# Performance work log

Hardware: AMD Instinct MI355X
Metric: run time of the kernel (lower is better)

The kernel has to match this reference:

```python
import jax, jax.numpy as jnp
import numpy as np

VARIANCES = jnp.array([0.1, 0.1, 0.2, 0.2], jnp.float32)
MAX_TOTAL = 200       # max_total_size
MAX_PER_CLASS = 50    # per-class NMS cap (combined-NMS max_output_size_per_class)
IOU_THR = 0.5
SCORE_THR = 0.5       # score_threshold
EPS = 1e-8


def setup_inputs() -> dict:
    key = jax.random.key(0)
    k1, k2, kc, kh = jax.random.split(key, 4)
    B, N, C = 16, 24564, 81
    pred_deltas = jax.random.normal(k1, (B, N, 4), jnp.float32)
    pred_labels = jax.random.uniform(k2, (B, N, C), jnp.float32)
    # realistic normalized priors: centers uniform in [0,1], sizes ~ [0.02, 0.22]
    ctr = jax.random.uniform(kc, (N, 2), jnp.float32)
    hw = jax.random.uniform(kh, (N, 2), jnp.float32) * 0.2 + 0.02
    y1x1 = jnp.clip(ctr - hw / 2, 0.0, 1.0)
    y2x2 = jnp.clip(ctr + hw / 2, 0.0, 1.0)
    prior_boxes = jnp.concatenate([y1x1, y2x2], axis=-1)  # (N,4) y1x1y2x2
    return {"pred_deltas": pred_deltas, "pred_labels": pred_labels, "prior_boxes": prior_boxes}


def _decode(deltas, priors):
    # deltas: (B,N,4) already scaled by variances; priors: (N,4) y1x1y2x2
    ph = priors[:, 2] - priors[:, 0]
    pw = priors[:, 3] - priors[:, 1]
    pcy = priors[:, 0] + 0.5 * ph
    pcx = priors[:, 1] + 0.5 * pw
    cy = deltas[..., 0] * ph + pcy
    cx = deltas[..., 1] * pw + pcx
    h = jnp.exp(deltas[..., 2]) * ph
    w = jnp.exp(deltas[..., 3]) * pw
    boxes = jnp.stack([cy - h / 2, cx - w / 2, cy + h / 2, cx + w / 2], axis=-1)
    return jnp.clip(boxes, 0.0, 1.0)  # combined NMS clip_boxes=True


def _iou_one_vs_all(box, boxes):
    # box: (4,), boxes: (N,4)
    iy1 = jnp.maximum(box[0], boxes[:, 0])
    ix1 = jnp.maximum(box[1], boxes[:, 1])
    iy2 = jnp.minimum(box[2], boxes[:, 2])
    ix2 = jnp.minimum(box[3], boxes[:, 3])
    inter = jnp.maximum(iy2 - iy1, 0.0) * jnp.maximum(ix2 - ix1, 0.0)
    a0 = (box[2] - box[0]) * (box[3] - box[1])
    a1 = (boxes[:, 2] - boxes[:, 0]) * (boxes[:, 3] - boxes[:, 1])
    return inter / (a0 + a1 - inter + EPS)


def _nms_indices(boxes, scores):
    # greedy NMS on one class: boxes (N,4), scores (N,) -> (K,) idx, (K,) valid
    def body(i, st):
        sc, idx, val = st
        j = jnp.argmax(sc)
        s = sc[j]
        iou = _iou_one_vs_all(boxes[j], boxes)
        sc = jnp.where(iou > IOU_THR, 0.0, sc).at[j].set(0.0)
        return sc, idx.at[i].set(j.astype(jnp.int32)), val.at[i].set(s > SCORE_THR)

    _, idx, val = jax.lax.fori_loop(
        0, MAX_PER_CLASS, body,
        (scores, jnp.zeros(MAX_PER_CLASS, jnp.int32), jnp.zeros(MAX_PER_CLASS, bool)))
    return idx, val


def reference(pred_deltas, pred_labels, prior_boxes):
    B = pred_deltas.shape[0]
    C = pred_labels.shape[-1]
    # 1) delta * variance scaling
    deltas = pred_deltas * VARIANCES
    # 2) background masking: zero all class scores where argmax class == 0
    lab_map = jnp.argmax(pred_labels, axis=-1, keepdims=True)  # (B,N,1)
    scores = jnp.where(lab_map != 0, pred_labels, jnp.zeros_like(pred_labels))  # (B,N,C)
    # 3) box decode (shared across classes, q=1)
    boxes = _decode(deltas, prior_boxes)  # (B,N,4)
    # 4) per-class greedy NMS (combined NMS)
    scores_cn = jnp.swapaxes(scores, 1, 2)  # (B,C,N)
    boxes_sg = jax.lax.stop_gradient(boxes)
    scores_sg = jax.lax.stop_gradient(scores_cn)
    per_class = jax.vmap(lambda bx, sc: jax.vmap(_nms_indices, in_axes=(None, 0))(bx, sc))
    idx, val = per_class(boxes_sg, scores_sg)  # (B,C,K) int32, (B,C,K) bool
    # 5) gather kept detections, merge across classes, keep global top MAX_TOTAL
    sel_scores = jnp.take_along_axis(scores_cn, idx, axis=2) * val  # (B,C,K)
    flat_scores = sel_scores.reshape(B, C * MAX_PER_CLASS)
    flat_idx = idx.reshape(B, C * MAX_PER_CLASS)
    top_scores, top_pos = jax.lax.top_k(flat_scores, MAX_TOTAL)  # (B,200)
    box_idx = jnp.take_along_axis(flat_idx, top_pos, axis=1)  # (B,200)
    sel_boxes = jnp.take_along_axis(boxes, box_idx[..., None], axis=1)  # (B,200,4)
    valid_mask = top_scores > 0.0
    sel_boxes = sel_boxes * valid_mask[..., None].astype(sel_boxes.dtype)
    sel_classes = (top_pos // MAX_PER_CLASS).astype(jnp.float32) * valid_mask
    valid_count = jnp.sum(valid_mask, axis=1).astype(jnp.int32)  # (B,)
    return sel_boxes, top_scores, sel_classes, valid_count
```

## Files before the change

### kernel.cpp

```cpp
#include <hip/hip_runtime.h>
#include <math.h>

#define BB 16
#define NN 24564
#define CC 81
#define KK 50
#define MT 200
#define NROWS (BB * NN)
#define PB2 768
#define CAND_CAP 512
#define T1 0.995f
#define T1C0 0.975f
#define TIER_W 0.02f
#define PADI 32
#define CHUNK 128

typedef unsigned long long u64;
typedef unsigned int u32;

__device__ __forceinline__ u64 pack_cand(float s, int n) {
    return ((u64)__float_as_uint(s) << 32) | (u32)(~(u32)n);
}

template <int P, int NT>
__device__ __forceinline__ void bitonic_desc(u64* a, int tid) {
    for (int k = 2; k <= P; k <<= 1) {
        for (int j = k >> 1; j > 0; j >>= 1) {
            for (int i = tid; i < P; i += NT) {
                int l = i ^ j;
                if (l > i) {
                    u64 x = a[i], y = a[l];
                    bool sw = (i & k) ? (x > y) : (x < y);
                    if (sw) { a[i] = y; a[l] = x; }
                }
            }
            __syncthreads();
        }
    }
}

__global__ __launch_bounds__(256) void k_zero(int* __restrict__ cnt_g)
{
    int i = blockIdx.x * 256 + threadIdx.x;
    if (i < BB * CC) cnt_g[i * PADI] = 0;
}

__global__ __launch_bounds__(128) void k_decode_filter(
    const float* __restrict__ deltas, const float* __restrict__ labels,
    const float* __restrict__ priors, float4* __restrict__ boxes,
    unsigned char* __restrict__ bg, int* __restrict__ cnt_g,
    u64* __restrict__ cand_g)
{
    __shared__ float4 lab4[648];
    __shared__ u64 s_mask[2][CC];
    __shared__ int s_base[2][CC];

    int tid = threadIdx.x;
    int w = tid >> 6, lane = tid & 63;
    int b = blockIdx.x / PB2, blk = blockIdx.x - b * PB2;
    int row0 = blk * 32;
    int rows = NN - row0; if (rows > 32) rows = 32;
    const float4* src = (const float4*)(labels + ((size_t)b * NN + row0) * CC);
    int nf4 = rows * CC / 4;

    int nfull = nf4 >> 6;
    for (int j = w; j < nfull; j += 2) {
        __builtin_amdgcn_global_load_lds(
            (const __attribute__((address_space(1))) void*)(src + (j << 6) + lane),
            (__attribute__((address_space(3))) void*)(lab4 + (j << 6)),
            16, 0, 0);
    }
    int idx = (nfull << 6) + tid;
    bool hasrem = idx < nf4;
    float4 tv;
    if (hasrem) tv = src[idx];
    asm volatile("s_waitcnt vmcnt(0)" ::: "memory");
    if (hasrem) lab4[idx] = tv;
    __syncthreads();

    int r16 = lane & 15, q = lane >> 4;
    int rl = w * 16 + r16;
    bool inb = rl < rows;
    int n = row0 + rl;
    const float* L = (const float*)lab4 + rl * CC;

    int c0 = (q == 0) ? 0 : 1 + q * 20;
    int nc = (q == 0) ? 21 : 20;
    float mq = L[c0];
    u32 win = 0;
    #pragma unroll
    for (int j = 0; j < 21; ++j) {
        if (j < nc) {
            float v = L[c0 + j];
            mq = fmaxf(mq, v);
            float th = (q == 0 && j == 0) ? T1C0 : T1;
            if (v > th) win |= 1u << j;
        }
    }
    float m = fmaxf(mq, __shfl_xor(mq, 16));
    m = fmaxf(m, __shfl_xor(m, 32));
    float L0 = L[0];
    bool isbg = (L0 >= m);
    if (inb && q == 0) bg[(size_t)b * NN + n] = isbg ? 1 : 0;
    if (!inb || isbg) win = 0;

    u64 w0; u32 w1;
    if (q == 0)      { w0 = win;             w1 = 0; }
    else if (q == 1) { w0 = (u64)win << 21;  w1 = 0; }
    else if (q == 2) { w0 = (u64)win << 41;  w1 = 0; }
    else             { w0 = (u64)win << 61;  w1 = win >> 3; }

    #pragma unroll 1
    for (int c = 0; c < 64; ++c) {
        u64 mm = __ballot((w0 >> c) & 1);
        if (lane == 0) s_mask[w][c] = mm;
    }
    #pragma unroll 1
    for (int c = 64; c < CC; ++c) {
        u64 mm = __ballot((w1 >> (c - 64)) & 1);
        if (lane == 0) s_mask[w][c] = mm;
    }

    {
        u64 mk = s_mask[w][lane];
        int v2 = 0;
        if (mk) v2 = atomicAdd(&cnt_g[(b * CC + lane) * PADI], (int)__popcll(mk));
        s_base[w][lane] = v2;
        int c3 = 64 + lane;
        if (c3 < CC) {
            u64 mk3 = s_mask[w][c3];
            int v3 = 0;
            if (mk3) v3 = atomicAdd(&cnt_g[(b * CC + c3) * PADI], (int)__popcll(mk3));
            s_base[w][c3] = v3;
        }
    }

    u64 ltmask = (lane == 63) ? 0x7FFFFFFFFFFFFFFFull : ((1ull << lane) - 1ull);
    u64 t0 = w0;
    while (t0) {
        int c = __ffsll(t0) - 1; t0 &= t0 - 1;
        u64 mm = s_mask[w][c];
        int p = s_base[w][c] + (int)__popcll(mm & ltmask);
        if (p < CAND_CAP)
            cand_g[(size_t)(b * CC + c) * CAND_CAP + p] = pack_cand(L[c], n);
    }
    u32 t1 = w1;
    while (t1) {
        int j = __ffs(t1) - 1; t1 &= t1 - 1;
        int c = 64 + j;
        u64 mm = s_mask[w][c];
        int p = s_base[w][c] + (int)__popcll(mm & ltmask);
        if (p < CAND_CAP)
            cand_g[(size_t)(b * CC + c) * CAND_CAP + p] = pack_cand(L[c], n);
    }

    if (inb && q == 0) {
        size_t r = (size_t)b * NN + n;
        float4 pr = ((const float4*)priors)[n];
        float ph  = __fsub_rn(pr.z, pr.x);
        float pw  = __fsub_rn(pr.w, pr.y);
        float pcy = __fadd_rn(pr.x, __fmul_rn(0.5f, ph));
        float pcx = __fadd_rn(pr.y, __fmul_rn(0.5f, pw));
        float4 dl = ((const float4*)deltas)[r];
        float d0 = __fmul_rn(dl.x, 0.1f);
        float d1 = __fmul_rn(dl.y, 0.1f);
        float d2 = __fmul_rn(dl.z, 0.2f);
        float d3 = __fmul_rn(dl.w, 0.2f);
        float cy = __fadd_rn(__fmul_rn(d0, ph), pcy);
        float cx = __fadd_rn(__fmul_rn(d1, pw), pcx);
        float hh = __fmul_rn(expf(d2), ph);
        float ww = __fmul_rn(expf(d3), pw);
        float h2 = __fmul_rn(hh, 0.5f);
        float w2 = __fmul_rn(ww, 0.5f);
        float y1 = fminf(fmaxf(__fsub_rn(cy, h2), 0.0f), 1.0f);
        float x1 = fminf(fmaxf(__fsub_rn(cx, w2), 0.0f), 1.0f);
        float y2 = fminf(fmaxf(__fadd_rn(cy, h2), 0.0f), 1.0f);
        float x2 = fminf(fmaxf(__fadd_rn(cx, w2), 0.0f), 1.0f);
        boxes[r] = make_float4(y1, x1, y2, x2);
    }
}

__global__ __launch_bounds__(256) void k_nms(
    const float* __restrict__ labels, const unsigned char* __restrict__ bg,
    const float4* __restrict__ boxes, const int* __restrict__ cnt_g,
    const u64* __restrict__ cand_g,
    float* __restrict__ out_s, int* __restrict__ out_i)
{
    __shared__ u64 arr[CAND_CAP];
    __shared__ float4 sbox[CHUNK];
    __shared__ float ks[KK];
    __shared__ int   ki[KK];
    __shared__ int s_kept, s_cnt;

    int bc = blockIdx.x, tid = threadIdx.x;
    int b = bc / CC, c = bc - b * CC;
    float thrc = (c == 0) ? T1C0 : T1;
    const float4* bxb = boxes + (size_t)b * NN;

    int gcnt = cnt_g[bc * PADI];
    bool ovf = gcnt > CAND_CAP;
    int cnt0 = ovf ? 0 : gcnt;
    for (int i = tid; i < CAND_CAP; i += 256)
        arr[i] = (i < cnt0) ? cand_g[(size_t)bc * CAND_CAP + i] : 0ull;
    if (tid == 0) { s_kept = 0; s_cnt = cnt0; }
    __syncthreads();

    float4 kb = make_float4(0.f, 0.f, 0.f, 0.f);
    float  ka = 0.0f;
    float hi = ovf ? 1.0001f : thrc;
    float bw = TIER_W;
    bool first = !ovf;

    while (true) {
        if (!first) {
            if (s_kept >= KK || hi <= 0.5f) break;
            float lo = fmaxf(hi - bw, 0.5f);
            if (tid == 0) s_cnt = 0;
            __syncthreads();
            const float* lab = labels + (size_t)b * NN * CC + c;
            const unsigned char* bgb = bg + (size_t)b * NN;
            for (int n = tid; n < NN; n += 256) {
                float v = lab[(size_t)n * CC];
                if (v > lo && v <= hi && v > 0.5f && !bgb[n]) {
                    int p = atomicAdd(&s_cnt, 1);
                    if (p < CAND_CAP) arr[p] = pack_cand(v, n);
                }
            }
            __syncthreads();
            if (s_cnt > CAND_CAP && bw > 1e-7f) {
                bw *= 0.5f;
                __syncthreads();
                continue;
            }
            int c2 = min(s_cnt, CAND_CAP);
            for (int i = tid; i < CAND_CAP; i += 256)
                if (i >= c2) arr[i] = 0ull;
            hi = lo;
            bw = TIER_W;
            __syncthreads();
        }
        first = false;

        int cs = min(s_cnt, CAND_CAP);
        if (cs <= 128)      bitonic_desc<128, 256>(arr, tid);
        else if (cs <= 256) bitonic_desc<256, 256>(arr, tid);
        else                bitonic_desc<CAND_CAP, 256>(arr, tid);

        for (int ch0 = 0; ch0 < cs; ch0 += CHUNK) {
            if (s_kept >= KK) break;
            int che = min(ch0 + CHUNK, cs);
            for (int i = ch0 + tid; i < che; i += 256) {
                int n = (int)(~(u32)arr[i]);
                if ((u32)n < (u32)NN) sbox[i - ch0] = bxb[n];
            }
            __syncthreads();
            if (tid < 64) {
                int kept = s_kept;
                for (int i = ch0; i < che; ++i) {
                    u64 key = arr[i];
                    float sc = __uint_as_float((u32)(key >> 32));
                    int n = (int)(~(u32)key);
                    float4 cb = sbox[i - ch0];
                    float a1 = __fmul_rn(__fsub_rn(cb.z, cb.x), __fsub_rn(cb.w, cb.y));
                    bool sup = false;
                    if (tid < kept) {
                        float iy1 = fmaxf(kb.x, cb.x);
                        float ix1 = fmaxf(kb.y, cb.y);
                        float iy2 = fminf(kb.z, cb.z);
                        float ix2 = fminf(kb.w, cb.w);
                        float ih = fmaxf(__fsub_rn(iy2, iy1), 0.0f);
                        float iw = fmaxf(__fsub_rn(ix2, ix1), 0.0f);
                        float inter = __fmul_rn(ih, iw);
                        float den = __fadd_rn(__fsub_rn(__fadd_rn(ka, a1), inter), 1e-8f);
                        sup = __fdiv_rn(inter, den) > 0.5f;
                    }
                    if (__ballot(sup) == 0ull) {
                        if (tid == kept) { kb = cb; ka = a1; }
                        if (tid == 0)    { ks[kept] = sc; ki[kept] = n; }
                        ++kept;
                        if (kept == KK) break;
                    }
                }
                if (tid == 0) s_kept = kept;
            }
            __syncthreads();
        }
    }

    int kept = min(s_kept, KK);
    for (int k = tid; k < KK; k += 256) {
        out_s[(size_t)bc * KK + k] = (k < kept) ? ks[k] : 0.0f;
        out_i[(size_t)bc * KK + k] = (k < kept) ? ki[k] : 0;
    }
}

__global__ __launch_bounds__(256) void k_topk1(
    const float* __restrict__ nms_s, u64* __restrict__ topA)
{
    __shared__ u64 arr[512];
    int bchunk = blockIdx.x;
    int b = bchunk >> 3, ch = bchunk & 7;
    int tid = threadIdx.x;
    int base = ch * 512;
    for (int i = tid; i < 512; i += 256) {
        int fp = base + i;
        u64 v = 0ull;
        if (fp < CC * KK) {
            float s = nms_s[(size_t)b * CC * KK + fp];
            v = ((u64)__float_as_uint(s) << 32) | (u32)(~(u32)fp);
        }
        arr[i] = v;
    }
    __syncthreads();
    bitonic_desc<512, 256>(arr, tid);
    if (tid < MT) topA[(size_t)bchunk * MT + tid] = arr[tid];
}

__global__ __launch_bounds__(512) void k_topk2(
    const u64* __restrict__ topA, const int* __restrict__ nms_i,
    const float4* __restrict__ boxes, float* __restrict__ out)
{
    __shared__ u64 arr[2048];
    __shared__ int s_vc;
    int b = blockIdx.x, tid = threadIdx.x;
    for (int i = tid; i < 2048; i += 512)
        arr[i] = (i < 8 * MT) ? topA[(size_t)b * 8 * MT + i] : 0ull;
    if (tid == 0) s_vc = 0;
    __syncthreads();

    bitonic_desc<2048, 512>(arr, tid);

    if (tid < MT) {
        u64 key = arr[tid];
        float sc = __uint_as_float((u32)(key >> 32));
        int fp = (int)(~(u32)key);
        bool valid = sc > 0.0f;
        float4 bb = make_float4(0.f, 0.f, 0.f, 0.f);
        float cls = 0.0f;
        if (valid) {
            int aidx = nms_i[(size_t)b * CC * KK + fp];
            bb = boxes[(size_t)b * NN + aidx];
            cls = (float)(fp / KK);
        }
        ((float4*)out)[(size_t)b * MT + tid] = bb;
        out[(size_t)BB * MT * 4 + (size_t)b * MT + tid] = sc;
        out[(size_t)BB * MT * 5 + (size_t)b * MT + tid] = cls;
        if (valid) atomicAdd(&s_vc, 1);
    }
    __syncthreads();
    if (tid == 0) out[(size_t)BB * MT * 6 + b] = (float)s_vc;
}

extern "C" void kernel_launch(void* const* d_in, const int* in_sizes, int n_in,
                              void* d_out, int out_size, void* d_ws, size_t ws_size,
                              hipStream_t stream)
{
    const float* deltas = (const float*)d_in[0];
    const float* labels = (const float*)d_in[1];
    const float* priors = (const float*)d_in[2];
    float* out = (float*)d_out;

    char* ws = (char*)d_ws;
    size_t off = 0;
    float4* boxes = (float4*)(ws + off);            off += (size_t)NROWS * 16;
    unsigned char* bg = (unsigned char*)(ws + off); off += ((size_t)NROWS + 127) & ~127ull;
    int* cnt_g = (int*)(ws + off);                  off += (size_t)BB * CC * PADI * 4;
    u64* cand_g = (u64*)(ws + off);                 off += (size_t)BB * CC * CAND_CAP * 8;
    float* nms_s = (float*)(ws + off);              off += (size_t)BB * CC * KK * 4;
    int* nms_i = (int*)(ws + off);                  off += (size_t)BB * CC * KK * 4;
    u64* topA = (u64*)(ws + off);                   off += (size_t)BB * 8 * MT * 8;

    k_zero<<<(BB * CC + 255) / 256, 256, 0, stream>>>(cnt_g);
    k_decode_filter<<<BB * PB2, 128, 0, stream>>>(deltas, labels, priors,
                                                  boxes, bg, cnt_g, cand_g);
    k_nms<<<BB * CC, 256, 0, stream>>>(labels, bg, boxes, cnt_g, cand_g, nms_s, nms_i);
    k_topk1<<<BB * 8, 256, 0, stream>>>(nms_s, topA);
    k_topk2<<<BB, 512, 0, stream>>>(topA, nms_i, boxes, out);
}
```

Baseline: 147.2 us.

## Process 64 rows per block and ballot only classes with candidates

Each decode/filter block now handles 64 rows instead of 32, with two lanes per row each scanning half of the classes instead of four lanes per row. A wave-wide OR reduction of the candidate bitmasks lets the ballot loop visit only classes that have candidates, rather than issuing 81 ballots unconditionally, and the shared masks are zeroed first. This cuts per-row ballot overhead and halves the block count, at the cost of a longer serial per-lane scan over 40 or 41 classes and a doubled LDS buffer, which may reduce occupancy.

New measurement: 137.9 us. -6.3%, faster.

```diff
diff --git a/kernel.cpp b/kernel.cpp
--- a/kernel.cpp
+++ b/kernel.cpp
@@ -7,7 +7,7 @@
 #define KK 50
 #define MT 200
 #define NROWS (BB * NN)
-#define PB2 768
+#define RB 384
 #define CAND_CAP 512
 #define T1 0.995f
 #define T1C0 0.975f
@@ -51,15 +51,15 @@
     unsigned char* __restrict__ bg, int* __restrict__ cnt_g,
     u64* __restrict__ cand_g)
 {
-    __shared__ float4 lab4[648];
+    __shared__ float4 lab4[1296];
     __shared__ u64 s_mask[2][CC];
     __shared__ int s_base[2][CC];
 
     int tid = threadIdx.x;
     int w = tid >> 6, lane = tid & 63;
-    int b = blockIdx.x / PB2, blk = blockIdx.x - b * PB2;
-    int row0 = blk * 32;
-    int rows = NN - row0; if (rows > 32) rows = 32;
+    int b = blockIdx.x / RB, blk = blockIdx.x - b * RB;
+    int row0 = blk * 64;
+    int rows = NN - row0; if (rows > 64) rows = 64;
     const float4* src = (const float4*)(labels + ((size_t)b * NN + row0) * CC);
     int nf4 = rows * CC / 4;
 
@@ -78,47 +78,51 @@
     if (hasrem) lab4[idx] = tv;
     __syncthreads();
 
-    int r16 = lane & 15, q = lane >> 4;
-    int rl = w * 16 + r16;
+    int row = lane & 31, h = lane >> 5;
+    int rl = w * 32 + row;
     bool inb = rl < rows;
     int n = row0 + rl;
     const float* L = (const float*)lab4 + rl * CC;
 
-    int c0 = (q == 0) ? 0 : 1 + q * 20;
-    int nc = (q == 0) ? 21 : 20;
+    int c0 = h ? 41 : 0, c1 = h ? 81 : 41;
+    float L0 = L[0];
     float mq = L[c0];
-    u32 win = 0;
+    u64 win = 0;
+    for (int c = c0; c < c1; ++c) {
+        float v = L[c];
+        mq = fmaxf(mq, v);
+        float th = (c == 0) ? T1C0 : T1;
+        if (v > th) win |= 1ull << (c - c0);
+    }
+    float rm = fmaxf(mq, __shfl_xor(mq, 32));
+    bool isbg = (L0 >= rm);
+    if (inb && h == 0) bg[(size_t)b * NN + n] = isbg ? 1 : 0;
+    if (!inb || isbg) win = 0;
+
+    u64 w0 = h ? (win << 41) : win;
+    u32 w1 = h ? (u32)(win >> 23) : 0u;
+
+    u64 u0 = w0; u32 u1 = w1;
     #pragma unroll
-    for (int j = 0; j < 21; ++j) {
-        if (j < nc) {
-            float v = L[c0 + j];
-            mq = fmaxf(mq, v);
-            float th = (q == 0 && j == 0) ? T1C0 : T1;
-            if (v > th) win |= 1u << j;
-        }
-    }
-    float m = fmaxf(mq, __shfl_xor(mq, 16));
-    m = fmaxf(m, __shfl_xor(m, 32));
-    float L0 = L[0];
-    bool isbg = (L0 >= m);
-    if (inb && q == 0) bg[(size_t)b * NN + n] = isbg ? 1 : 0;
-    if (!inb || isbg) win = 0;
-
-    u64 w0; u32 w1;
-    if (q == 0)      { w0 = win;             w1 = 0; }
-    else if (q == 1) { w0 = (u64)win << 21;  w1 = 0; }
-    else if (q == 2) { w0 = (u64)win << 41;  w1 = 0; }
-    else             { w0 = (u64)win << 61;  w1 = win >> 3; }
-
-    #pragma unroll 1
-    for (int c = 0; c < 64; ++c) {
+    for (int off = 1; off < 64; off <<= 1) {
+        u0 |= __shfl_xor(u0, off);
+        u1 |= __shfl_xor(u1, off);
+    }
+
+    s_mask[w][lane] = 0ull;
+    if (lane < CC - 64) s_mask[w][64 + lane] = 0ull;
+
+    u64 t0u = u0;
+    while (t0u) {
+        int c = __ffsll(t0u) - 1; t0u &= t0u - 1;
         u64 mm = __ballot((w0 >> c) & 1);
         if (lane == 0) s_mask[w][c] = mm;
     }
-    #pragma unroll 1
-    for (int c = 64; c < CC; ++c) {
-        u64 mm = __ballot((w1 >> (c - 64)) & 1);
-        if (lane == 0) s_mask[w][c] = mm;
+    u32 t1u = u1;
+    while (t1u) {
+        int j = __ffs(t1u) - 1; t1u &= t1u - 1;
+        u64 mm = __ballot((w1 >> j) & 1);
+        if (lane == 0) s_mask[w][64 + j] = mm;
     }
 
     {
@@ -136,25 +140,18 @@
     }
 
     u64 ltmask = (lane == 63) ? 0x7FFFFFFFFFFFFFFFull : ((1ull << lane) - 1ull);
-    u64 t0 = w0;
-    while (t0) {
-        int c = __ffsll(t0) - 1; t0 &= t0 - 1;
+    u64 wrem = win;
+    while (wrem) {
+        int j = __ffsll(wrem) - 1;
+        wrem &= wrem - 1;
+        int c = h * 41 + j;
         u64 mm = s_mask[w][c];
         int p = s_base[w][c] + (int)__popcll(mm & ltmask);
         if (p < CAND_CAP)
             cand_g[(size_t)(b * CC + c) * CAND_CAP + p] = pack_cand(L[c], n);
     }
-    u32 t1 = w1;
-    while (t1) {
-        int j = __ffs(t1) - 1; t1 &= t1 - 1;
-        int c = 64 + j;
-        u64 mm = s_mask[w][c];
-        int p = s_base[w][c] + (int)__popcll(mm & ltmask);
-        if (p < CAND_CAP)
-            cand_g[(size_t)(b * CC + c) * CAND_CAP + p] = pack_cand(L[c], n);
-    }
-
-    if (inb && q == 0) {
+
+    if (inb && h == 0) {
         size_t r = (size_t)b * NN + n;
         float4 pr = ((const float4*)priors)[n];
         float ph  = __fsub_rn(pr.z, pr.x);
@@ -371,8 +368,8 @@
     u64* topA = (u64*)(ws + off);                   off += (size_t)BB * 8 * MT * 8;
 
     k_zero<<<(BB * CC + 255) / 256, 256, 0, stream>>>(cnt_g);
-    k_decode_filter<<<BB * PB2, 128, 0, stream>>>(deltas, labels, priors,
-                                                  boxes, bg, cnt_g, cand_g);
+    k_decode_filter<<<BB * RB, 128, 0, stream>>>(deltas, labels, priors,
+                                                 boxes, bg, cnt_g, cand_g);
     k_nms<<<BB * CC, 256, 0, stream>>>(labels, bg, boxes, cnt_g, cand_g, nms_s, nms_i);
     k_topk1<<<BB * 8, 256, 0, stream>>>(nms_s, topA);
     k_topk2<<<BB, 512, 0, stream>>>(topA, nms_i, boxes, out);
```
